# Kernel tuning notes

Measured on AMD Instinct MI355X. Metric: run time of the kernel, lower is better.

The kernel has to match this reference:

```python
import jax, jax.numpy as jnp
import numpy as np

CONV_K = 4
C_EXP = 8.0  # Griffin exponent constant
EPS = 1.1920929e-07  # torch RMSNorm default eps = finfo(float32).eps


def rmsnorm(x, w):
    return x * jax.lax.rsqrt(jnp.mean(x * x, axis=-1, keepdims=True) + EPS) * w


def gelu(x):
    return jax.nn.gelu(x, approximate=False)  # torch F.gelu default (erf)


def setup_inputs() -> dict:
    B, T, D = 16, 1024, 1024
    H = 4 * D  # GatedMLP hidden
    key = jax.random.key(0)
    ks = jax.random.split(key, 16)
    s = 0.02
    return {
        "x_seq": jax.random.normal(ks[0], (B, T, D), jnp.float32),
        "h0": jnp.zeros((B, D), jnp.float32),
        "conv_buf": jax.random.normal(ks[1], (B, CONV_K - 1, D), jnp.float32),
        "norm1_w": jnp.ones((D,), jnp.float32),
        "W1": jax.random.normal(ks[2], (D, D), jnp.float32) * s,
        "conv_w": jax.random.normal(ks[3], (D, CONV_K), jnp.float32) * s,
        "conv_b": jnp.zeros((D,), jnp.float32),
        "Wa": jax.random.normal(ks[4], (D, D), jnp.float32) * s,
        "ba": jnp.zeros((D,), jnp.float32),
        "Wx": jax.random.normal(ks[5], (D, D), jnp.float32) * s,
        "bx": jnp.zeros((D,), jnp.float32),
        "log_lambda": jnp.linspace(0.0, 4.0, D).astype(jnp.float32),
        "W2": jax.random.normal(ks[6], (D, D), jnp.float32) * s,
        "Wout": jax.random.normal(ks[7], (D, D), jnp.float32) * s,
        "norm2_w": jnp.ones((D,), jnp.float32),
        "Wg": jax.random.normal(ks[8], (H, D), jnp.float32) * s,
        "Wu": jax.random.normal(ks[9], (H, D), jnp.float32) * s,
        "Wo": jax.random.normal(ks[10], (D, H), jnp.float32) * s,
    }


def _block(x_seq, h0, conv_buf, norm1_w, W1, conv_w, conv_b, Wa, ba, Wx, bx,
           log_lambda, W2, Wout, norm2_w, Wg, Wu, Wo):
    B, T, D = x_seq.shape
    normed = rmsnorm(x_seq, norm1_w)
    b1 = normed @ W1.T                                   # (B,T,D)
    padded = jnp.concatenate([conv_buf, b1], axis=1)     # (B,T+3,D)
    # depthwise causal conv (cross-correlation, matching torch Conv1d)
    b1_conv = conv_b
    for k in range(CONV_K):
        b1_conv = b1_conv + padded[:, k:k + T, :] * conv_w[:, k]
    new_conv_buf = padded[:, -(CONV_K - 1):, :]

    # RG-LRU: precompute gates, scan only the diagonal linear recurrence
    r = jax.nn.sigmoid(b1_conv @ Wa.T + ba)
    i = jax.nn.sigmoid(b1_conv @ Wx.T + bx)
    a = jnp.exp((C_EXP * r) * jax.nn.log_sigmoid(log_lambda))  # sigmoid(L)**(c*r)
    gate = jnp.sqrt(jnp.clip((1.0 - a) * (1.0 + a), 1e-06))
    u = gate * (i * b1_conv)

    def step(h, au):
        a_t, u_t = au
        h = a_t * h + u_t
        return h, h

    new_h, outs = jax.lax.scan(step, h0,
                               (jnp.swapaxes(a, 0, 1), jnp.swapaxes(u, 0, 1)))
    b1_out = jnp.swapaxes(outs, 0, 1)                    # (B,T,D)

    b2 = gelu(normed @ W2.T)
    recurrent_out = (b1_out * b2) @ Wout.T
    x1 = x_seq + recurrent_out

    n2 = rmsnorm(x1, norm2_w)
    mlp = (gelu(n2 @ Wg.T) * (n2 @ Wu.T)) @ Wo.T         # GeGLU gated MLP
    x2 = x1 + mlp
    return x2, new_h, new_conv_buf


def reference(x_seq, h0, conv_buf, norm1_w, W1, conv_w, conv_b, Wa, ba, Wx, bx,
              log_lambda, W2, Wout, norm2_w, Wg, Wu, Wo):
    return _block(x_seq, h0, conv_buf, norm1_w, W1, conv_w, conv_b, Wa, ba,
                  Wx, bx, log_lambda, W2, Wout, norm2_w, Wg, Wu, Wo)
```

## Files before the change

kernel.cpp:

```cpp
#include <hip/hip_runtime.h>
#include <hip/hip_bf16.h>
#include <cstdint>

using bf16 = __hip_bfloat16;
typedef __attribute__((ext_vector_type(8))) short bf16x8;
typedef __attribute__((ext_vector_type(4))) float f32x4;

#define NB 16
#define NT_ 1024
#define ND 1024
#define NH 4096
#define NM (NB * NT_)

enum { EPI_BF16 = 0, EPI_OM, EPI_U, EPI_GELU, EPI_GELU_MUL, EPI_X1, EPI_X2 };

__device__ __forceinline__ float sigm(float x) { return 1.0f / (1.0f + expf(-x)); }
__device__ __forceinline__ float gelu_f(float x) { return 0.5f * x * (1.0f + erff(x * 0.7071067811865476f)); }
__device__ __forceinline__ float b2f(bf16 h) { return __bfloat162float(h); }
__device__ __forceinline__ bf16  f2b(float x) { return __float2bfloat16(x); }

__device__ __forceinline__ void gl_lds16(const bf16* g, void* l) {
  __builtin_amdgcn_global_load_lds((const __attribute__((address_space(1))) void*)g,
                                   (__attribute__((address_space(3))) void*)l, 16, 0, 0);
}

template <int EPI>
__global__ __launch_bounds__(256)
void gemm_nt(const bf16* __restrict__ A, const bf16* __restrict__ Bw,
             int M, int N, int K,
             const float* __restrict__ biasf, const float* __restrict__ vecf,
             const bf16* __restrict__ auxb, const bf16* __restrict__ auxb2,
             const float* __restrict__ auxf,
             float* __restrict__ outf, bf16* __restrict__ outb)
{
  __shared__ __align__(16) bf16 As[128 * 32];
  __shared__ __align__(16) bf16 Bs[128 * 32];
  const int tid  = threadIdx.x;
  const int wave = tid >> 6, lane = tid & 63;
  const int lr = lane & 15, lq = lane >> 4;
  const int m0 = blockIdx.y * 128, n0 = blockIdx.x * 128;
  const int wm = (wave & 1) * 64, wn = (wave >> 1) * 64;

  f32x4 acc[4][4];
#pragma unroll
  for (int i = 0; i < 4; ++i)
#pragma unroll
    for (int j = 0; j < 4; ++j)
#pragma unroll
      for (int r = 0; r < 4; ++r) acc[i][j][r] = 0.0f;

  const bf16* Ab = A  + (long)m0 * K;
  const bf16* Bb = Bw + (long)n0 * K;
  const int row0 = tid >> 2;
  const int kp0  = (tid & 3) << 3;

  for (int k0 = 0; k0 < K; k0 += 32) {
    __syncthreads();
    gl_lds16(Ab + (long)row0 * K + k0 + kp0,        ((char*)As) + tid * 16);
    gl_lds16(Bb + (long)row0 * K + k0 + kp0,        ((char*)Bs) + tid * 16);
    gl_lds16(Ab + (long)(row0 + 64) * K + k0 + kp0, ((char*)As) + (tid + 256) * 16);
    gl_lds16(Bb + (long)(row0 + 64) * K + k0 + kp0, ((char*)Bs) + (tid + 256) * 16);
    __syncthreads();

    bf16x8 af[4], bfr[4];
#pragma unroll
    for (int i = 0; i < 4; ++i)
      af[i] = *reinterpret_cast<const bf16x8*>(&As[(wm + i * 16 + lr) * 32 + lq * 8]);
#pragma unroll
    for (int j = 0; j < 4; ++j)
      bfr[j] = *reinterpret_cast<const bf16x8*>(&Bs[(wn + j * 16 + lr) * 32 + lq * 8]);
#pragma unroll
    for (int i = 0; i < 4; ++i)
#pragma unroll
      for (int j = 0; j < 4; ++j)
        acc[i][j] = __builtin_amdgcn_mfma_f32_16x16x32_bf16(af[i], bfr[j], acc[i][j], 0, 0, 0);
  }

#pragma unroll
  for (int i = 0; i < 4; ++i) {
#pragma unroll
    for (int j = 0; j < 4; ++j) {
#pragma unroll
      for (int r = 0; r < 4; ++r) {
        const int row = m0 + wm + i * 16 + lq * 4 + r;
        const int col = n0 + wn + j * 16 + lr;
        const long idx = (long)row * N + col;
        float v = acc[i][j][r];
        if constexpr (EPI == EPI_BF16) {
          outb[idx] = f2b(v);
        } else if constexpr (EPI == EPI_OM) {
          float rr = sigm(v + biasf[col]);
          float ls = -log1pf(expf(-vecf[col]));
          outb[idx] = f2b(-expm1f(8.0f * rr * ls));
        } else if constexpr (EPI == EPI_U) {
          float ii = sigm(v + biasf[col]);
          float om = b2f(auxb2[idx]);
          float g  = sqrtf(fmaxf(om * (2.0f - om), 1e-6f));
          outb[idx] = f2b(g * ii * b2f(auxb[idx]));
        } else if constexpr (EPI == EPI_GELU) {
          outb[idx] = f2b(gelu_f(v));
        } else if constexpr (EPI == EPI_GELU_MUL) {
          float u2 = b2f(outb[idx]);
          outb[idx] = f2b(gelu_f(v) * u2);
        } else if constexpr (EPI == EPI_X1) {
          outb[idx] = f2b(v + auxf[idx]);
        } else if constexpr (EPI == EPI_X2) {
          outf[idx] = v + b2f(auxb[idx]);
        }
      }
    }
  }
}

__global__ __launch_bounds__(256)
void cast4_kernel(const float* __restrict__ in, bf16* __restrict__ out, long n4) {
  long i = (long)blockIdx.x * 256 + threadIdx.x;
  if (i < n4) {
    float4 v = reinterpret_cast<const float4*>(in)[i];
    union { bf16 h[4]; ushort4 u; } pk;
    pk.h[0] = f2b(v.x); pk.h[1] = f2b(v.y); pk.h[2] = f2b(v.z); pk.h[3] = f2b(v.w);
    reinterpret_cast<ushort4*>(out)[i] = pk.u;
  }
}

template <typename TIN>
__global__ __launch_bounds__(256)
void rmsnorm_kernel(const TIN* __restrict__ x, const float* __restrict__ w,
                    bf16* __restrict__ out) {
  const int row = blockIdx.x;
  const int t = threadIdx.x;
  float4 v;
  if constexpr (sizeof(TIN) == 4) {
    v = reinterpret_cast<const float4*>(x + (long)row * ND)[t];
  } else {
    union { ushort4 u; bf16 h[4]; } xv;
    xv.u = reinterpret_cast<const ushort4*>(x + (long)row * ND)[t];
    v = make_float4(b2f(xv.h[0]), b2f(xv.h[1]), b2f(xv.h[2]), b2f(xv.h[3]));
  }
  float ss = v.x * v.x + v.y * v.y + v.z * v.z + v.w * v.w;
#pragma unroll
  for (int off = 32; off > 0; off >>= 1) ss += __shfl_down(ss, off, 64);
  __shared__ float red[4];
  if ((t & 63) == 0) red[t >> 6] = ss;
  __syncthreads();
  float tot = red[0] + red[1] + red[2] + red[3];
  float scale = rsqrtf(tot * (1.0f / ND) + 1.1920929e-07f);
  float4 wv = reinterpret_cast<const float4*>(w)[t];
  union { bf16 h[4]; ushort4 u; } pk;
  pk.h[0] = f2b(v.x * scale * wv.x);
  pk.h[1] = f2b(v.y * scale * wv.y);
  pk.h[2] = f2b(v.z * scale * wv.z);
  pk.h[3] = f2b(v.w * scale * wv.w);
  reinterpret_cast<ushort4*>(out + (long)row * ND)[t] = pk.u;
}

__global__ __launch_bounds__(256)
void conv_kernel(const bf16* __restrict__ b1, const float* __restrict__ conv_buf,
                 const float* __restrict__ conv_w, const float* __restrict__ conv_b,
                 bf16* __restrict__ out_b1c, float* __restrict__ out_newbuf) {
  const long gid = (long)blockIdx.x * 256 + threadIdx.x;
  const int d = (int)(gid & (ND - 1));
  const long bt = gid >> 10;
  const int t = (int)(bt & (NT_ - 1));
  const int b = (int)(bt >> 10);
  float acc = conv_b[d];
#pragma unroll
  for (int k = 0; k < 4; ++k) {
    const int p = t + k;
    float src = (p < 3) ? conv_buf[((long)b * 3 + p) * ND + d]
                        : b2f(b1[((long)b * NT_ + (p - 3)) * ND + d]);
    acc = fmaf(conv_w[d * 4 + k], src, acc);
  }
  out_b1c[gid] = f2b(acc);
  if (t >= NT_ - 3)
    out_newbuf[((long)b * 3 + (t - (NT_ - 3))) * ND + d] = b2f(b1[gid]);
}

__global__ __launch_bounds__(256)
void scan_kernel(const bf16* __restrict__ om, const bf16* __restrict__ u,
                 const bf16* __restrict__ b2, const float* __restrict__ h0,
                 bf16* __restrict__ prod, float* __restrict__ newh) {
  const int gid = blockIdx.x * 256 + threadIdx.x;
  const int d = gid & (ND - 1);
  const int b = gid >> 10;
  float h = h0[gid];
  const long base = (long)b * NT_ * ND + d;
#pragma unroll 8
  for (int t = 0; t < NT_; ++t) {
    const long idx = base + (long)t * ND;
    h = fmaf(-b2f(om[idx]), h, h) + b2f(u[idx]);
    prod[idx] = f2b(h * b2f(b2[idx]));
  }
  newh[gid] = h;
}

extern "C" void kernel_launch(void* const* d_in, const int* in_sizes, int n_in,
                              void* d_out, int out_size, void* d_ws, size_t ws_size,
                              hipStream_t stream) {
  const float* x_seq    = (const float*)d_in[0];
  const float* h0       = (const float*)d_in[1];
  const float* conv_buf = (const float*)d_in[2];
  const float* norm1_w  = (const float*)d_in[3];
  const float* W1       = (const float*)d_in[4];
  const float* conv_w   = (const float*)d_in[5];
  const float* conv_b   = (const float*)d_in[6];
  const float* Wa       = (const float*)d_in[7];
  const float* ba       = (const float*)d_in[8];
  const float* Wx       = (const float*)d_in[9];
  const float* bx       = (const float*)d_in[10];
  const float* loglam   = (const float*)d_in[11];
  const float* W2       = (const float*)d_in[12];
  const float* Wout     = (const float*)d_in[13];
  const float* norm2_w  = (const float*)d_in[14];
  const float* Wg       = (const float*)d_in[15];
  const float* Wu       = (const float*)d_in[16];
  const float* Wo       = (const float*)d_in[17];

  char* ws = (char*)d_ws;
  bf16* normed = (bf16*)(ws);
  bf16* b1buf  = (bf16*)(ws + (32L  << 20));
  bf16* b1cbuf = (bf16*)(ws + (64L  << 20));
  bf16* Woutb  = (bf16*)(ws + (64L  << 20));
  bf16* ombuf  = (bf16*)(ws + (96L  << 20));
  bf16* ubuf   = (bf16*)(ws + (128L << 20));
  bf16* x1buf  = (bf16*)(ws + (160L << 20));
  bf16* b2buf  = x1buf;
  bf16* bigbuf = (bf16*)(ws + (32L  << 20));
  bf16* W1b    = (bf16*)(ws + (192L << 20));
  bf16* Wab    = (bf16*)(ws + (194L << 20));
  bf16* Wxb    = (bf16*)(ws + (196L << 20));
  bf16* W2b    = (bf16*)(ws + (198L << 20));
  bf16* Wgb    = (bf16*)(ws + (200L << 20));
  bf16* Wub    = (bf16*)(ws + (208L << 20));
  bf16* Wob    = (bf16*)(ws + (216L << 20));

  float* out_x2 = (float*)d_out;
  float* out_h  = out_x2 + (long)NM * ND;
  float* out_cb = out_h + NB * ND;

  const dim3 blk(256);
  const dim3 gD(ND / 128, NM / 128);
  const dim3 gH(NH / 128, NM / 128);

  cast4_kernel<<<dim3(1024), blk, 0, stream>>>(W1, W1b, 262144);
  cast4_kernel<<<dim3(1024), blk, 0, stream>>>(Wa, Wab, 262144);
  cast4_kernel<<<dim3(1024), blk, 0, stream>>>(Wx, Wxb, 262144);
  cast4_kernel<<<dim3(1024), blk, 0, stream>>>(W2, W2b, 262144);
  cast4_kernel<<<dim3(4096), blk, 0, stream>>>(Wg, Wgb, 1048576);
  cast4_kernel<<<dim3(4096), blk, 0, stream>>>(Wu, Wub, 1048576);
  cast4_kernel<<<dim3(4096), blk, 0, stream>>>(Wo, Wob, 1048576);

  rmsnorm_kernel<float><<<dim3(NM), blk, 0, stream>>>(x_seq, norm1_w, normed);
  gemm_nt<EPI_BF16><<<gD, blk, 0, stream>>>(normed, W1b, NM, ND, ND,
      nullptr, nullptr, nullptr, nullptr, nullptr, nullptr, b1buf);
  conv_kernel<<<dim3((NM * ND) / 256), blk, 0, stream>>>(b1buf, conv_buf, conv_w, conv_b,
      b1cbuf, out_cb);
  gemm_nt<EPI_OM><<<gD, blk, 0, stream>>>(b1cbuf, Wab, NM, ND, ND,
      ba, loglam, nullptr, nullptr, nullptr, nullptr, ombuf);
  gemm_nt<EPI_U><<<gD, blk, 0, stream>>>(b1cbuf, Wxb, NM, ND, ND,
      bx, nullptr, b1cbuf, ombuf, nullptr, nullptr, ubuf);
  gemm_nt<EPI_GELU><<<gD, blk, 0, stream>>>(normed, W2b, NM, ND, ND,
      nullptr, nullptr, nullptr, nullptr, nullptr, nullptr, b2buf);
  scan_kernel<<<dim3(NB * ND / 256), blk, 0, stream>>>(ombuf, ubuf, b2buf, h0, b1buf, out_h);
  cast4_kernel<<<dim3(1024), blk, 0, stream>>>(Wout, Woutb, 262144);
  gemm_nt<EPI_X1><<<gD, blk, 0, stream>>>(b1buf, Woutb, NM, ND, ND,
      nullptr, nullptr, nullptr, nullptr, x_seq, nullptr, x1buf);
  rmsnorm_kernel<bf16><<<dim3(NM), blk, 0, stream>>>(x1buf, norm2_w, normed);
  gemm_nt<EPI_BF16><<<gH, blk, 0, stream>>>(normed, Wub, NM, NH, ND,
      nullptr, nullptr, nullptr, nullptr, nullptr, nullptr, bigbuf);
  gemm_nt<EPI_GELU_MUL><<<gH, blk, 0, stream>>>(normed, Wgb, NM, NH, ND,
      nullptr, nullptr, nullptr, nullptr, nullptr, nullptr, bigbuf);
  gemm_nt<EPI_X2><<<gD, blk, 0, stream>>>(bigbuf, Wob, NM, ND, NH,
      nullptr, nullptr, x1buf, nullptr, nullptr, out_x2, nullptr);
}
```

Measured before the change: 1.407 ms.

## Replace GEMM with 256x256-tile double-buffered pipelined MFMA kernel

Replaces the simple 128x128, BK=32, single-buffered GEMM with a 512-thread kernel that computes 256x256 output tiles using BK=64. It double-buffers LDS (128KB) with async global-to-LDS loads interleaved between MFMA phases, uses XOR-swizzled LDS layout to avoid bank conflicts, s_setprio around MFMA bursts, and a grid-swizzled block mapping for L2 locality. This targets the LDS bandwidth, load latency and sync stalls of the old kernel, at the cost of a large LDS footprint limiting occupancy and complex wait-count logic that relies on exact counts of outstanding loads.

```diff
diff --git a/kernel.cpp b/kernel.cpp
--- a/kernel.cpp
+++ b/kernel.cpp
@@ -25,65 +25,140 @@
 }
 
 template <int EPI>
-__global__ __launch_bounds__(256)
-void gemm_nt(const bf16* __restrict__ A, const bf16* __restrict__ Bw,
+__global__ __launch_bounds__(512, 2)
+void gemm256(const bf16* __restrict__ A, const bf16* __restrict__ Bw,
              int M, int N, int K,
              const float* __restrict__ biasf, const float* __restrict__ vecf,
              const bf16* __restrict__ auxb, const bf16* __restrict__ auxb2,
              const float* __restrict__ auxf,
              float* __restrict__ outf, bf16* __restrict__ outb)
 {
-  __shared__ __align__(16) bf16 As[128 * 32];
-  __shared__ __align__(16) bf16 Bs[128 * 32];
-  const int tid  = threadIdx.x;
+  (void)M;
+  __shared__ __align__(16) char lds[131072];
+  const int tid  = (int)threadIdx.x;
   const int wave = tid >> 6, lane = tid & 63;
   const int lr = lane & 15, lq = lane >> 4;
-  const int m0 = blockIdx.y * 128, n0 = blockIdx.x * 128;
-  const int wm = (wave & 1) * 64, wn = (wave >> 1) * 64;
-
-  f32x4 acc[4][4];
-#pragma unroll
-  for (int i = 0; i < 4; ++i)
+  const int wm = wave >> 2, wn = wave & 3;
+
+  const int nwg = (int)gridDim.x;
+  const int swz = ((int)blockIdx.x & 7) * (nwg >> 3) + ((int)blockIdx.x >> 3);
+  const int nbx = N >> 8;
+  const int by = swz / nbx, bx = swz - by * nbx;
+  const int m0 = by << 8, n0 = bx << 8;
+  const int NT = K >> 6;
+
+  const bf16* __restrict__ Ag = A  + (long)m0 * K;
+  const bf16* __restrict__ Bg = Bw + (long)n0 * K;
+
+  const int lrow = lane >> 2;
+  const int kbs  = (lane & 3) ^ (((lane >> 5) & 1) << 1);
+  const int rswz   = (lq * 16) ^ ((lr & 8) << 2);
+  const int aRdOff = wm * 8192 + lr * 64 + rswz;
+  const int bRdOff = 32768 + wn * 4096 + lr * 64 + rswz;
+
+#define STAGE_A(T, H, BUF) do { \
+  _Pragma("unroll") for (int n2_ = 0; n2_ < 2; ++n2_) { \
+    const int cc_ = wave * 2 + n2_, kh_ = cc_ >> 3, r0_ = (cc_ & 7) << 4; \
+    gl_lds16(Ag + (long)((H) * 128 + r0_ + lrow) * K + ((T) * 64 + kh_ * 32 + kbs * 8), \
+             lds + (BUF) * 65536 + kh_ * 16384 + ((H) * 128 + r0_) * 64 + lane * 16); } } while (0)
+#define STAGE_B(T, H, BUF) do { \
+  _Pragma("unroll") for (int n2_ = 0; n2_ < 2; ++n2_) { \
+    const int cc_ = wave * 2 + n2_, kh_ = cc_ >> 3, r0_ = (cc_ & 7) << 4; \
+    gl_lds16(Bg + (long)((H) * 128 + r0_ + lrow) * K + ((T) * 64 + kh_ * 32 + kbs * 8), \
+             lds + (BUF) * 65536 + 32768 + kh_ * 16384 + ((H) * 128 + r0_) * 64 + lane * 16); } } while (0)
+
+  f32x4 acc[8][4];
+#pragma unroll
+  for (int i = 0; i < 8; ++i)
 #pragma unroll
     for (int j = 0; j < 4; ++j)
 #pragma unroll
       for (int r = 0; r < 4; ++r) acc[i][j][r] = 0.0f;
 
-  const bf16* Ab = A  + (long)m0 * K;
-  const bf16* Bb = Bw + (long)n0 * K;
-  const int row0 = tid >> 2;
-  const int kp0  = (tid & 3) << 3;
-
-  for (int k0 = 0; k0 < K; k0 += 32) {
-    __syncthreads();
-    gl_lds16(Ab + (long)row0 * K + k0 + kp0,        ((char*)As) + tid * 16);
-    gl_lds16(Bb + (long)row0 * K + k0 + kp0,        ((char*)Bs) + tid * 16);
-    gl_lds16(Ab + (long)(row0 + 64) * K + k0 + kp0, ((char*)As) + (tid + 256) * 16);
-    gl_lds16(Bb + (long)(row0 + 64) * K + k0 + kp0, ((char*)Bs) + (tid + 256) * 16);
-    __syncthreads();
-
-    bf16x8 af[4], bfr[4];
-#pragma unroll
-    for (int i = 0; i < 4; ++i)
-      af[i] = *reinterpret_cast<const bf16x8*>(&As[(wm + i * 16 + lr) * 32 + lq * 8]);
-#pragma unroll
-    for (int j = 0; j < 4; ++j)
-      bfr[j] = *reinterpret_cast<const bf16x8*>(&Bs[(wn + j * 16 + lr) * 32 + lq * 8]);
-#pragma unroll
-    for (int i = 0; i < 4; ++i)
-#pragma unroll
-      for (int j = 0; j < 4; ++j)
-        acc[i][j] = __builtin_amdgcn_mfma_f32_16x16x32_bf16(af[i], bfr[j], acc[i][j], 0, 0, 0);
-  }
-
-#pragma unroll
-  for (int i = 0; i < 4; ++i) {
+  STAGE_B(0, 0, 0); STAGE_B(0, 1, 0); STAGE_A(0, 0, 0); STAGE_A(0, 1, 0);
+  STAGE_B(1, 0, 1); STAGE_B(1, 1, 1); STAGE_A(1, 0, 1);
+  asm volatile("s_waitcnt vmcnt(6)" ::: "memory");
+  __builtin_amdgcn_s_barrier();
+
+  bf16x8 bF[4][2], aF[2][2], aG[2][2];
+
+#define RD(P, OFF) (*(const bf16x8*)((P) + (OFF)))
+#define MFMA_I(IS, A0, A1) do { \
+  _Pragma("unroll") for (int j_ = 0; j_ < 4; ++j_) { \
+    acc[IS][j_] = __builtin_amdgcn_mfma_f32_16x16x32_bf16((A0), bF[j_][0], acc[IS][j_], 0, 0, 0); \
+    acc[IS][j_] = __builtin_amdgcn_mfma_f32_16x16x32_bf16((A1), bF[j_][1], acc[IS][j_], 0, 0, 0); } } while (0)
+
+#define TILE(T, CUR) do { \
+    const char* Ap_ = lds + (CUR) * 65536; \
+     \
+    _Pragma("unroll") for (int j_ = 0; j_ < 4; ++j_) { \
+      bF[j_][0] = RD(Ap_, bRdOff + j_ * 1024); \
+      bF[j_][1] = RD(Ap_, bRdOff + 16384 + j_ * 1024); } \
+    aF[0][0] = RD(Ap_, aRdOff);          aF[0][1] = RD(Ap_, aRdOff + 16384); \
+    aF[1][0] = RD(Ap_, aRdOff + 1024);   aF[1][1] = RD(Ap_, aRdOff + 16384 + 1024); \
+    if ((T) + 1 < NT) STAGE_A((T) + 1, 1, (CUR) ^ 1); \
+    __builtin_amdgcn_s_barrier(); \
+    asm volatile("s_waitcnt lgkmcnt(0)" ::: "memory"); \
+    __builtin_amdgcn_s_setprio(1); \
+    MFMA_I(0, aF[0][0], aF[0][1]); \
+    MFMA_I(1, aF[1][0], aF[1][1]); \
+    __builtin_amdgcn_s_setprio(0); \
+    __builtin_amdgcn_s_barrier(); \
+     \
+    aF[0][0] = RD(Ap_, aRdOff + 2 * 1024); aF[0][1] = RD(Ap_, aRdOff + 16384 + 2 * 1024); \
+    aF[1][0] = RD(Ap_, aRdOff + 3 * 1024); aF[1][1] = RD(Ap_, aRdOff + 16384 + 3 * 1024); \
+    if ((T) + 2 < NT) STAGE_B((T) + 2, 0, (CUR)); \
+    __builtin_amdgcn_s_barrier(); \
+    asm volatile("s_waitcnt lgkmcnt(0)" ::: "memory"); \
+    __builtin_amdgcn_s_setprio(1); \
+    MFMA_I(2, aF[0][0], aF[0][1]); \
+    MFMA_I(3, aF[1][0], aF[1][1]); \
+    __builtin_amdgcn_s_setprio(0); \
+    __builtin_amdgcn_s_barrier(); \
+     \
+    aF[0][0] = RD(Ap_, aRdOff + 4 * 1024); aF[0][1] = RD(Ap_, aRdOff + 16384 + 4 * 1024); \
+    aF[1][0] = RD(Ap_, aRdOff + 5 * 1024); aF[1][1] = RD(Ap_, aRdOff + 16384 + 5 * 1024); \
+    aG[0][0] = RD(Ap_, aRdOff + 6 * 1024); aG[0][1] = RD(Ap_, aRdOff + 16384 + 6 * 1024); \
+    aG[1][0] = RD(Ap_, aRdOff + 7 * 1024); aG[1][1] = RD(Ap_, aRdOff + 16384 + 7 * 1024); \
+    if ((T) + 2 < NT) STAGE_B((T) + 2, 1, (CUR)); \
+    __builtin_amdgcn_s_barrier(); \
+    asm volatile("s_waitcnt lgkmcnt(0)" ::: "memory"); \
+    __builtin_amdgcn_s_setprio(1); \
+    MFMA_I(4, aF[0][0], aF[0][1]); \
+    MFMA_I(5, aF[1][0], aF[1][1]); \
+    __builtin_amdgcn_s_setprio(0); \
+    __builtin_amdgcn_s_barrier(); \
+     \
+    if ((T) + 2 < NT) STAGE_A((T) + 2, 0, (CUR)); \
+    __builtin_amdgcn_s_barrier(); \
+    asm volatile("s_waitcnt lgkmcnt(0)" ::: "memory"); \
+    __builtin_amdgcn_s_setprio(1); \
+    MFMA_I(6, aG[0][0], aG[0][1]); \
+    MFMA_I(7, aG[1][0], aG[1][1]); \
+    __builtin_amdgcn_s_setprio(0); \
+    if ((T) + 2 < NT)      { asm volatile("s_waitcnt vmcnt(6)" ::: "memory"); } \
+    else if ((T) + 1 < NT) { asm volatile("s_waitcnt vmcnt(0)" ::: "memory"); } \
+    __builtin_amdgcn_s_barrier(); \
+  } while (0)
+
+  for (int t = 0; t < NT; t += 2) {
+    TILE(t, 0);
+    TILE(t + 1, 1);
+  }
+#undef TILE
+#undef MFMA_I
+#undef RD
+#undef STAGE_A
+#undef STAGE_B
+
+#pragma unroll
+  for (int i = 0; i < 8; ++i) {
 #pragma unroll
     for (int j = 0; j < 4; ++j) {
 #pragma unroll
       for (int r = 0; r < 4; ++r) {
-        const int row = m0 + wm + i * 16 + lq * 4 + r;
-        const int col = n0 + wn + j * 16 + lr;
+        const int row = m0 + wm * 128 + i * 16 + lq * 4 + r;
+        const int col = n0 + wn * 64 + j * 16 + lr;
         const long idx = (long)row * N + col;
         float v = acc[i][j][r];
         if constexpr (EPI == EPI_BF16) {
@@ -239,8 +314,9 @@
   float* out_cb = out_h + NB * ND;
 
   const dim3 blk(256);
-  const dim3 gD(ND / 128, NM / 128);
-  const dim3 gH(NH / 128, NM / 128);
+  const dim3 blk512(512);
+  const dim3 gD256((NM / 256) * (ND / 256));
+  const dim3 gH256((NM / 256) * (NH / 256));
 
   cast4_kernel<<<dim3(1024), blk, 0, stream>>>(W1, W1b, 262144);
   cast4_kernel<<<dim3(1024), blk, 0, stream>>>(Wa, Wab, 262144);
@@ -251,25 +327,25 @@
   cast4_kernel<<<dim3(4096), blk, 0, stream>>>(Wo, Wob, 1048576);
 
   rmsnorm_kernel<float><<<dim3(NM), blk, 0, stream>>>(x_seq, norm1_w, normed);
-  gemm_nt<EPI_BF16><<<gD, blk, 0, stream>>>(normed, W1b, NM, ND, ND,
+  gemm256<EPI_BF16><<<gD256, blk512, 0, stream>>>(normed, W1b, NM, ND, ND,
       nullptr, nullptr, nullptr, nullptr, nullptr, nullptr, b1buf);
   conv_kernel<<<dim3((NM * ND) / 256), blk, 0, stream>>>(b1buf, conv_buf, conv_w, conv_b,
       b1cbuf, out_cb);
-  gemm_nt<EPI_OM><<<gD, blk, 0, stream>>>(b1cbuf, Wab, NM, ND, ND,
+  gemm256<EPI_OM><<<gD256, blk512, 0, stream>>>(b1cbuf, Wab, NM, ND, ND,
       ba, loglam, nullptr, nullptr, nullptr, nullptr, ombuf);
-  gemm_nt<EPI_U><<<gD, blk, 0, stream>>>(b1cbuf, Wxb, NM, ND, ND,
+  gemm256<EPI_U><<<gD256, blk512, 0, stream>>>(b1cbuf, Wxb, NM, ND, ND,
       bx, nullptr, b1cbuf, ombuf, nullptr, nullptr, ubuf);
-  gemm_nt<EPI_GELU><<<gD, blk, 0, stream>>>(normed, W2b, NM, ND, ND,
+  gemm256<EPI_GELU><<<gD256, blk512, 0, stream>>>(normed, W2b, NM, ND, ND,
       nullptr, nullptr, nullptr, nullptr, nullptr, nullptr, b2buf);
   scan_kernel<<<dim3(NB * ND / 256), blk, 0, stream>>>(ombuf, ubuf, b2buf, h0, b1buf, out_h);
   cast4_kernel<<<dim3(1024), blk, 0, stream>>>(Wout, Woutb, 262144);
-  gemm_nt<EPI_X1><<<gD, blk, 0, stream>>>(b1buf, Woutb, NM, ND, ND,
+  gemm256<EPI_X1><<<gD256, blk512, 0, stream>>>(b1buf, Woutb, NM, ND, ND,
       nullptr, nullptr, nullptr, nullptr, x_seq, nullptr, x1buf);
   rmsnorm_kernel<bf16><<<dim3(NM), blk, 0, stream>>>(x1buf, norm2_w, normed);
-  gemm_nt<EPI_BF16><<<gH, blk, 0, stream>>>(normed, Wub, NM, NH, ND,
+  gemm256<EPI_BF16><<<gH256, blk512, 0, stream>>>(normed, Wub, NM, NH, ND,
       nullptr, nullptr, nullptr, nullptr, nullptr, nullptr, bigbuf);
-  gemm_nt<EPI_GELU_MUL><<<gH, blk, 0, stream>>>(normed, Wgb, NM, NH, ND,
+  gemm256<EPI_GELU_MUL><<<gH256, blk512, 0, stream>>>(normed, Wgb, NM, NH, ND,
       nullptr, nullptr, nullptr, nullptr, nullptr, nullptr, bigbuf);
-  gemm_nt<EPI_X2><<<gD, blk, 0, stream>>>(bigbuf, Wob, NM, ND, NH,
+  gemm256<EPI_X2><<<gD256, blk512, 0, stream>>>(bigbuf, Wob, NM, ND, NH,
       nullptr, nullptr, x1buf, nullptr, nullptr, out_x2, nullptr);
 }
```

Result: faster. 1.135 ms (-19.3%).
